# Optimization experiments

Hardware: AMD Instinct MI355X
Metric: run time of the kernel (lower is better)

The kernel has to match this reference:

```python
import jax, jax.numpy as jnp
import numpy as np

B, S, E, H = 2, 2048, 1024, 16
D = E // H  # head_dim = 64

def setup_inputs() -> dict:
    key = jax.random.key(0)
    ks = jax.random.split(key, 11)
    s = 1.0 / np.sqrt(E)
    inp = {
        'query': jax.random.normal(ks[0], (B, S, E), jnp.float32),
        'key':   jax.random.normal(ks[1], (B, S, E), jnp.float32),
        'value': jax.random.normal(ks[2], (B, S, E), jnp.float32),
        'Wq': jax.random.uniform(ks[3], (E, E), jnp.float32, -s, s),
        'bq': jax.random.uniform(ks[4], (E,), jnp.float32, -s, s),
        'Wk': jax.random.uniform(ks[5], (E, E), jnp.float32, -s, s),
        'bk': jax.random.uniform(ks[6], (E,), jnp.float32, -s, s),
        'Wv': jax.random.uniform(ks[7], (E, E), jnp.float32, -s, s),
        'bv': jax.random.uniform(ks[8], (E,), jnp.float32, -s, s),
        'Wo': jax.random.uniform(ks[9], (E, E), jnp.float32, -s, s),
        'bo': jax.random.uniform(ks[10], (E,), jnp.float32, -s, s),
    }
    return inp

def reference(query, key, value, Wq, bq, Wk, bk, Wv, bv, Wo, bo):
    # project and split heads: [B,S,E] -> [B,H,S,D]
    def proj(x, W, b):
        y = jnp.einsum('bse,fe->bsf', x, W) + b  # torch Linear: x @ W.T + b
        return y.reshape(B, S, H, D).transpose(0, 2, 1, 3)
    q = proj(query, Wq, bq)
    k = proj(key, Wk, bk)
    v = proj(value, Wv, bv)
    scores = jnp.einsum('bhqd,bhkd->bhqk', q, k) / jnp.sqrt(jnp.float32(D))
    attn = jax.nn.softmax(scores, axis=-1)
    out = jnp.einsum('bhqk,bhkd->bhqd', attn, v)  # [B,H,S,D]
    out = out.transpose(0, 2, 1, 3).reshape(B, S, E)
    return jnp.einsum('bse,fe->bsf', out, Wo) + bo
```

## Files before the change

kernel.cpp:

```cpp
#include <hip/hip_runtime.h>

#define B_ 2
#define S_ 2048
#define E_ 1024
#define H_ 16
#define D_ 64
#define M_ (B_*S_)
#define K_ E_

typedef __attribute__((ext_vector_type(8))) short  short8;
typedef __attribute__((ext_vector_type(4))) float  f32x4;
typedef __attribute__((ext_vector_type(8))) unsigned short u16x8;
typedef __attribute__((ext_vector_type(4))) unsigned short u16x4;
typedef __attribute__((ext_vector_type(4))) unsigned int   u32x4;

#define QSCALE 0.18033688011112042f

#if __has_builtin(__builtin_amdgcn_exp2f)
#define EXP2F(x) __builtin_amdgcn_exp2f(x)
#else
#define EXP2F(x) exp2f(x)
#endif

__device__ __forceinline__ unsigned short f2bf(float f) {
    unsigned u = __float_as_uint(f);
    u += 0x7fffu + ((u >> 16) & 1u);
    return (unsigned short)(u >> 16);
}

__device__ __forceinline__ void gl_lds16(const ushort* g, ushort* l) {
    __builtin_amdgcn_global_load_lds((const __attribute__((address_space(1))) void*)g,
                                     (__attribute__((address_space(3))) void*)l,
                                     16, 0, 0);
}

__global__ __launch_bounds__(256)
void cvt_all(const float* __restrict__ q, const float* __restrict__ k,
             const float* __restrict__ v, const float* __restrict__ wq,
             const float* __restrict__ wk, const float* __restrict__ wv,
             const float* __restrict__ wo, ushort* __restrict__ dst)
{
    const int bid = blockIdx.x;
    const float* src;
    size_t dof;
    int local;
    if (bid < 6144) {
        const int t = bid >> 11;
        src = (t == 0) ? q : (t == 1) ? k : v;
        dof = (size_t)t * 4194304u;
        local = bid & 2047;
    } else {
        const int r = bid - 6144;
        const int t = r >> 9;
        src = (t == 0) ? wq : (t == 1) ? wk : (t == 2) ? wv : wo;
        dof = 12582912u + (size_t)t * 1048576u;
        local = r & 511;
    }
    const size_t idx = (size_t)local * 2048 + threadIdx.x * 8;
    const float4 a = *(const float4*)(src + idx);
    const float4 b = *(const float4*)(src + idx + 4);
    u16x8 o;
    o[0] = f2bf(a.x); o[1] = f2bf(a.y); o[2] = f2bf(a.z); o[3] = f2bf(a.w);
    o[4] = f2bf(b.x); o[5] = f2bf(b.y); o[6] = f2bf(b.z); o[7] = f2bf(b.w);
    *(u16x8*)(dst + dof + idx) = o;
}

template<int SWAP>
__device__ __forceinline__ void gemm_core(const ushort* __restrict__ X,
                                          const ushort* __restrict__ W,
                                          int m0, int n0,
                                          f32x4 acc[4][4],
                                          ushort* Ast, ushort* Bst)
{
    const int tid  = threadIdx.x;
    const int lane = tid & 63;
    const int w    = tid >> 6;
    const int wm   = w & 1, wn = w >> 1;
    const int r0   = tid >> 2;
    const int c8   = (tid & 3) * 8;

    const f32x4 zero = {0.f, 0.f, 0.f, 0.f};
    #pragma unroll
    for (int mt = 0; mt < 4; ++mt)
        #pragma unroll
        for (int nt = 0; nt < 4; ++nt) acc[mt][nt] = zero;

    const int kb = (lane >> 4) * 8;

    for (int k0 = 0; k0 < K_; k0 += 32) {
        __syncthreads();
        const ushort* ga = X + (size_t)(m0 + r0) * K_ + k0 + c8;
        gl_lds16(ga, Ast + tid * 8);
        gl_lds16(ga + (size_t)64 * K_, Ast + 2048 + tid * 8);
        const ushort* gb = W + (size_t)(n0 + r0) * K_ + k0 + c8;
        gl_lds16(gb, Bst + tid * 8);
        gl_lds16(gb + (size_t)64 * K_, Bst + 2048 + tid * 8);
        __syncthreads();

        short8 af[4], bf[4];
        #pragma unroll
        for (int mt = 0; mt < 4; ++mt)
            af[mt] = *(const short8*)(Ast + (wm * 64 + mt * 16 + (lane & 15)) * 32 + kb);
        #pragma unroll
        for (int nt = 0; nt < 4; ++nt)
            bf[nt] = *(const short8*)(Bst + (wn * 64 + nt * 16 + (lane & 15)) * 32 + kb);
        #pragma unroll
        for (int mt = 0; mt < 4; ++mt)
            #pragma unroll
            for (int nt = 0; nt < 4; ++nt) {
                if (SWAP)
                    acc[mt][nt] = __builtin_amdgcn_mfma_f32_16x16x32_bf16(bf[nt], af[mt], acc[mt][nt], 0, 0, 0);
                else
                    acc[mt][nt] = __builtin_amdgcn_mfma_f32_16x16x32_bf16(af[mt], bf[nt], acc[mt][nt], 0, 0, 0);
            }
    }
}

__global__ __launch_bounds__(256)
void gemm_qkv(const ushort* __restrict__ Xq, const ushort* __restrict__ Xk,
              const ushort* __restrict__ Xv, const ushort* __restrict__ Wq,
              const ushort* __restrict__ Wk, const ushort* __restrict__ Wv,
              const float* __restrict__ bq, const float* __restrict__ bk,
              const float* __restrict__ bv, ushort* __restrict__ Qh,
              ushort* __restrict__ Kh, ushort* __restrict__ Vt)
{
    __shared__ ushort Ast[128 * 32];
    __shared__ ushort Bst[128 * 32];
    const int z = blockIdx.z;
    const ushort* X = (z == 0) ? Xq : (z == 1) ? Xk : Xv;
    const ushort* W = (z == 0) ? Wq : (z == 1) ? Wk : Wv;
    const float* bias = (z == 0) ? bq : (z == 1) ? bk : bv;
    ushort* dst = (z == 0) ? Qh : (z == 1) ? Kh : Vt;

    const int m0 = blockIdx.y * 128, n0 = blockIdx.x * 128;
    f32x4 acc[4][4];
    const int lane = threadIdx.x & 63, w = threadIdx.x >> 6;
    const int wm = w & 1, wn = w >> 1;
    const int l15 = lane & 15, quad = lane >> 4;

    if (z < 2) {
        gemm_core<1>(X, W, m0, n0, acc, Ast, Bst);
        const float qsc = (z == 0) ? QSCALE : 1.0f;
        #pragma unroll
        for (int nt = 0; nt < 4; ++nt) {
            const int nb = n0 + wn * 64 + nt * 16 + quad * 4;
            const int h = nb >> 6, d0 = nb & 63;
            const float4 b4 = *(const float4*)(bias + nb);
            const float bb4[4] = {b4.x, b4.y, b4.z, b4.w};
            #pragma unroll
            for (int mt = 0; mt < 4; ++mt) {
                const int tok = m0 + wm * 64 + mt * 16 + l15;
                const int b = tok >> 11, s = tok & (S_ - 1);
                u16x4 pk;
                #pragma unroll
                for (int r = 0; r < 4; ++r)
                    pk[r] = f2bf((acc[mt][nt][r] + bb4[r]) * qsc);
                *(u16x4*)&dst[(((size_t)(b * H_ + h) * S_) + s) * D_ + d0] = pk;
            }
        }
    } else {
        gemm_core<0>(X, W, m0, n0, acc, Ast, Bst);
        float bias4[4];
        #pragma unroll
        for (int nt = 0; nt < 4; ++nt)
            bias4[nt] = bias[n0 + wn * 64 + nt * 16 + l15];
        #pragma unroll
        for (int mt = 0; mt < 4; ++mt) {
            const int mrow0 = m0 + wm * 64 + mt * 16 + (quad * 4);
            const int b = mrow0 >> 11;
            const int s0 = mrow0 & (S_ - 1);
            #pragma unroll
            for (int nt = 0; nt < 4; ++nt) {
                const int n = n0 + wn * 64 + nt * 16 + l15;
                const int h = n >> 6, d = n & 63;
                u16x4 pk;
                #pragma unroll
                for (int r = 0; r < 4; ++r) pk[r] = f2bf(acc[mt][nt][r] + bias4[nt]);
                *(u16x4*)&Vt[(((size_t)(b * H_ + h) * D_) + d) * S_ + s0] = pk;
            }
        }
    }
}

__global__ __launch_bounds__(256)
void gemm_out(const ushort* __restrict__ X, const ushort* __restrict__ W,
              const float* __restrict__ bias, float* __restrict__ out)
{
    __shared__ ushort Ast[128 * 32];
    __shared__ ushort Bst[64 * 32];
    const int m0 = blockIdx.y * 128, n0 = blockIdx.x * 64;
    const int tid = threadIdx.x, lane = tid & 63, w = tid >> 6;
    const int wm = w & 1, wn = w >> 1;
    const int l15 = lane & 15, quad = lane >> 4;
    const int r0 = tid >> 2, c8 = (tid & 3) * 8;
    const int kb = quad * 8;

    const f32x4 zero = {0.f, 0.f, 0.f, 0.f};
    f32x4 acc[4][2];
    #pragma unroll
    for (int mt = 0; mt < 4; ++mt)
        #pragma unroll
        for (int nt = 0; nt < 2; ++nt) acc[mt][nt] = zero;

    for (int k0 = 0; k0 < K_; k0 += 32) {
        __syncthreads();
        const ushort* ga = X + (size_t)(m0 + r0) * K_ + k0 + c8;
        gl_lds16(ga, Ast + tid * 8);
        gl_lds16(ga + (size_t)64 * K_, Ast + 2048 + tid * 8);
        const ushort* gb = W + (size_t)(n0 + r0) * K_ + k0 + c8;
        gl_lds16(gb, Bst + tid * 8);
        __syncthreads();

        short8 af[4], bf[2];
        #pragma unroll
        for (int mt = 0; mt < 4; ++mt)
            af[mt] = *(const short8*)(Ast + (wm * 64 + mt * 16 + l15) * 32 + kb);
        #pragma unroll
        for (int nt = 0; nt < 2; ++nt)
            bf[nt] = *(const short8*)(Bst + (wn * 32 + nt * 16 + l15) * 32 + kb);
        #pragma unroll
        for (int mt = 0; mt < 4; ++mt)
            #pragma unroll
            for (int nt = 0; nt < 2; ++nt)
                acc[mt][nt] = __builtin_amdgcn_mfma_f32_16x16x32_bf16(af[mt], bf[nt], acc[mt][nt], 0, 0, 0);
    }

    float bias2[2];
    #pragma unroll
    for (int nt = 0; nt < 2; ++nt)
        bias2[nt] = bias[n0 + wn * 32 + nt * 16 + l15];

    #pragma unroll
    for (int mt = 0; mt < 4; ++mt) {
        const int mrow0 = m0 + wm * 64 + mt * 16 + quad * 4;
        #pragma unroll
        for (int nt = 0; nt < 2; ++nt) {
            const int n = n0 + wn * 32 + nt * 16 + l15;
            #pragma unroll
            for (int r = 0; r < 4; ++r)
                out[(size_t)(mrow0 + r) * E_ + n] = acc[mt][nt][r] + bias2[nt];
        }
    }
}

#define NTILE (S_ / 64)
__global__ __launch_bounds__(256, 3)
void flash_mfma(const ushort* __restrict__ Qg, const ushort* __restrict__ Kg,
                const ushort* __restrict__ Vg, ushort* __restrict__ AO)
{
    __shared__ ushort sh[20480];
    ushort* Qs = sh;
    ushort* K0 = sh + 4096;
    ushort* V0 = sh + 8192;
    ushort* K1 = sh + 12288;
    ushort* V1 = sh + 16384;

    const int tid = threadIdx.x, lane = tid & 63, w = tid >> 6;
    const int l15 = lane & 15, quad = lane >> 4;
    const int q0 = blockIdx.x * 64, h = blockIdx.y, b = blockIdx.z;
    const size_t qk_off = (size_t)(b * H_ + h) * S_ * D_;
    const size_t vt_off = (size_t)(b * H_ + h) * D_ * S_;

    #pragma unroll
    for (int i = 0; i < 2; ++i) {
        const int chunk = w + i * 4;
        const int row = chunk * 8 + (lane >> 3);
        const int gcol = (lane & 7) ^ (row & 7);
        gl_lds16(Qg + qk_off + (size_t)(q0 + row) * D_ + gcol * 8,
                 Qs + chunk * 512 + lane * 8);
        gl_lds16(Kg + qk_off + (size_t)row * D_ + gcol * 8,
                 K0 + chunk * 512 + lane * 8);
        gl_lds16(Vg + vt_off + (size_t)row * S_ + gcol * 8,
                 V0 + chunk * 512 + lane * 8);
    }
    __syncthreads();

    const f32x4 zero = {0.f, 0.f, 0.f, 0.f};
    f32x4 o[4][4];
    #pragma unroll
    for (int g = 0; g < 4; ++g)
        #pragma unroll
        for (int nt = 0; nt < 4; ++nt) o[g][nt] = zero;
    float lsum[4] = {0.f, 0.f, 0.f, 0.f};

    const int krow = (w * 16 + l15) * 64;
    const int gidx = (2 * w + (quad >> 1)) ^ (l15 & 7);

    for (int jp = 0; jp < NTILE; jp += 2) {
        short8 ka[2];
        #pragma unroll
        for (int kt = 0; kt < 2; ++kt)
            ka[kt] = *(const short8*)&K0[krow + (((kt * 4 + quad) ^ (l15 & 7)) * 8)];
        uint2 vvA[4];
        #pragma unroll
        for (int nt = 0; nt < 4; ++nt)
            vvA[nt] = *(const uint2*)&V0[(nt * 16 + l15) * 64 + gidx * 8 + (quad & 1) * 4];

        {
            const int j0n = (jp + 1) * 64;
            #pragma unroll
            for (int i = 0; i < 2; ++i) {
                const int chunk = w + i * 4;
                const int row = chunk * 8 + (lane >> 3);
                const int gcol = (lane & 7) ^ (row & 7);
                gl_lds16(Kg + qk_off + (size_t)(j0n + row) * D_ + gcol * 8,
                         K1 + chunk * 512 + lane * 8);
                gl_lds16(Vg + vt_off + (size_t)row * S_ + j0n + gcol * 8,
                         V1 + chunk * 512 + lane * 8);
            }
        }

        uint2 paLo[4];
        #pragma unroll
        for (int g = 0; g < 4; ++g) {
            const short8 qg0 = *(const short8*)&Qs[(g * 16 + l15) * 64 +
                                                   ((quad ^ (l15 & 7)) * 8)];
            const short8 qg1 = *(const short8*)&Qs[(g * 16 + l15) * 64 +
                                                   (((4 + quad) ^ (l15 & 7)) * 8)];
            f32x4 t;
            t = __builtin_amdgcn_mfma_f32_16x16x32_bf16(ka[0], qg0, zero, 0, 0, 0);
            t = __builtin_amdgcn_mfma_f32_16x16x32_bf16(ka[1], qg1, t, 0, 0, 0);
            const float p0 = EXP2F(t[0]), p1 = EXP2F(t[1]);
            const float p2 = EXP2F(t[2]), p3 = EXP2F(t[3]);
            lsum[g] += (p0 + p1) + (p2 + p3);
            const unsigned a0 = __float_as_uint(p0) + 0x8000u;
            const unsigned a1 = __float_as_uint(p1) + 0x8000u;
            const unsigned a2 = __float_as_uint(p2) + 0x8000u;
            const unsigned a3 = __float_as_uint(p3) + 0x8000u;
            paLo[g].x = (a1 & 0xffff0000u) | (a0 >> 16);
            paLo[g].y = (a3 & 0xffff0000u) | (a2 >> 16);
        }
        __syncthreads();

        #pragma unroll
        for (int kt = 0; kt < 2; ++kt)
            ka[kt] = *(const short8*)&K1[krow + (((kt * 4 + quad) ^ (l15 & 7)) * 8)];
        uint2 vvB[4];
        #pragma unroll
        for (int nt = 0; nt < 4; ++nt)
            vvB[nt] = *(const uint2*)&V1[(nt * 16 + l15) * 64 + gidx * 8 + (quad & 1) * 4];

        if (jp + 2 < NTILE) {
            const int j0n = (jp + 2) * 64;
            #pragma unroll
            for (int i = 0; i < 2; ++i) {
                const int chunk = w + i * 4;
                const int row = chunk * 8 + (lane >> 3);
                const int gcol = (lane & 7) ^ (row & 7);
                gl_lds16(Kg + qk_off + (size_t)(j0n + row) * D_ + gcol * 8,
                         K0 + chunk * 512 + lane * 8);
                gl_lds16(Vg + vt_off + (size_t)row * S_ + j0n + gcol * 8,
                         V0 + chunk * 512 + lane * 8);
            }
        }

        short8 pa8[4];
        #pragma unroll
        for (int g = 0; g < 4; ++g) {
            const short8 qg0 = *(const short8*)&Qs[(g * 16 + l15) * 64 +
                                                   ((quad ^ (l15 & 7)) * 8)];
            const short8 qg1 = *(const short8*)&Qs[(g * 16 + l15) * 64 +
                                                   (((4 + quad) ^ (l15 & 7)) * 8)];
            f32x4 t;
            t = __builtin_amdgcn_mfma_f32_16x16x32_bf16(ka[0], qg0, zero, 0, 0, 0);
            t = __builtin_amdgcn_mfma_f32_16x16x32_bf16(ka[1], qg1, t, 0, 0, 0);
            const float p0 = EXP2F(t[0]), p1 = EXP2F(t[1]);
            const float p2 = EXP2F(t[2]), p3 = EXP2F(t[3]);
            lsum[g] += (p0 + p1) + (p2 + p3);
            const unsigned a0 = __float_as_uint(p0) + 0x8000u;
            const unsigned a1 = __float_as_uint(p1) + 0x8000u;
            const unsigned a2 = __float_as_uint(p2) + 0x8000u;
            const unsigned a3 = __float_as_uint(p3) + 0x8000u;
            u32x4 pk;
            pk[0] = paLo[g].x;
            pk[1] = paLo[g].y;
            pk[2] = (a1 & 0xffff0000u) | (a0 >> 16);
            pk[3] = (a3 & 0xffff0000u) | (a2 >> 16);
            pa8[g] = __builtin_bit_cast(short8, pk);
        }

        #pragma unroll
        for (int nt = 0; nt < 4; ++nt) {
            u32x4 vk;
            vk[0] = vvA[nt].x; vk[1] = vvA[nt].y;
            vk[2] = vvB[nt].x; vk[3] = vvB[nt].y;
            const short8 vb8 = __builtin_bit_cast(short8, vk);
            #pragma unroll
            for (int g = 0; g < 4; ++g)
                o[g][nt] = __builtin_amdgcn_mfma_f32_16x16x32_bf16(pa8[g], vb8, o[g][nt], 0, 0, 0);
        }

        __syncthreads();
    }

    #pragma unroll
    for (int g = 0; g < 4; ++g) {
        lsum[g] += __shfl_xor(lsum[g], 16);
        lsum[g] += __shfl_xor(lsum[g], 32);
    }
    __syncthreads();
    float* fb = (float*)sh;
    #pragma unroll
    for (int g = 0; g < 4; ++g) {
        if (w != g) {
            #pragma unroll
            for (int nt = 0; nt < 4; ++nt)
                #pragma unroll
                for (int r = 0; r < 4; ++r)
                    fb[w * 1024 + (nt * 4 + r) * 64 + lane] = o[g][nt][r];
            if (quad == 0) fb[4096 + w * 64 + l15] = lsum[g];
        }
        __syncthreads();
        if (w == g) {
            #pragma unroll
            for (int ws = 0; ws < 4; ++ws) {
                if (ws == g) continue;
                #pragma unroll
                for (int nt = 0; nt < 4; ++nt)
                    #pragma unroll
                    for (int r = 0; r < 4; ++r)
                        o[g][nt][r] += fb[ws * 1024 + (nt * 4 + r) * 64 + lane];
                lsum[g] += fb[4096 + ws * 64 + l15];
            }
        }
        __syncthreads();
    }

    #pragma unroll
    for (int g = 0; g < 4; ++g) {
        if (w == g) {
            const float inv = 1.0f / lsum[g];
            float invr[4];
            #pragma unroll
            for (int r = 0; r < 4; ++r)
                invr[r] = __shfl(inv, (lane & 0x30) | (quad * 4 + r));
            #pragma unroll
            for (int nt = 0; nt < 4; ++nt) {
                const int e = h * 64 + nt * 16 + l15;
                #pragma unroll
                for (int r = 0; r < 4; ++r) {
                    const int s = q0 + g * 16 + quad * 4 + r;
                    AO[(size_t)(b * S_ + s) * E_ + e] = f2bf(o[g][nt][r] * invr[r]);
                }
            }
        }
    }
}

extern "C" void kernel_launch(void* const* d_in, const int* in_sizes, int n_in,
                              void* d_out, int out_size, void* d_ws, size_t ws_size,
                              hipStream_t stream) {
    const float* query = (const float*)d_in[0];
    const float* key   = (const float*)d_in[1];
    const float* value = (const float*)d_in[2];
    const float* Wq = (const float*)d_in[3];
    const float* bq = (const float*)d_in[4];
    const float* Wk = (const float*)d_in[5];
    const float* bk = (const float*)d_in[6];
    const float* Wv = (const float*)d_in[7];
    const float* bv = (const float*)d_in[8];
    const float* Wo = (const float*)d_in[9];
    const float* bo = (const float*)d_in[10];
    float* out = (float*)d_out;

    ushort* ws = (ushort*)d_ws;
    ushort* Xq  = ws;
    ushort* Xk  = ws + 4194304u;
    ushort* Xv  = ws + 8388608u;
    ushort* Wqb = ws + 12582912u;
    ushort* Wkb = ws + 13631488u;
    ushort* Wvb = ws + 14680064u;
    ushort* Wob = ws + 15728640u;
    ushort* Qh  = ws + 16777216u;
    ushort* Kh  = ws + 20971520u;
    ushort* Vt  = ws + 25165824u;
    ushort* AO  = ws + 29360128u;

    cvt_all<<<8192, 256, 0, stream>>>(query, key, value, Wq, Wk, Wv, Wo, ws);
    gemm_qkv<<<dim3(8, 32, 3), 256, 0, stream>>>(Xq, Xk, Xv, Wqb, Wkb, Wvb,
                                                 bq, bk, bv, Qh, Kh, Vt);
    flash_mfma<<<dim3(32, 16, 2), 256, 0, stream>>>(Qh, Kh, Vt, AO);
    gemm_out<<<dim3(16, 32), 256, 0, stream>>>(AO, Wob, bo, out);
}
```

Baseline: 232.5 us.

## Deepen flash attention K/V pipeline to four LDS stages with vmcnt barriers

Replaces the double-buffered K/V prefetch in the flash attention kernel with a four-stage ring buffer in LDS, issuing loads three tiles ahead. __syncthreads is replaced by explicit s_waitcnt vmcnt(N) plus s_barrier, so only the oldest stage has to land before compute. Q fragments are hoisted into registers once instead of being reread from LDS every tile. LDS use grows to about 72KB and launch bounds drop to 2 blocks per CU, which trades occupancy for deeper latency hiding.

```diff
diff --git a/kernel.cpp b/kernel.cpp
--- a/kernel.cpp
+++ b/kernel.cpp
@@ -33,6 +33,12 @@
                                      (__attribute__((address_space(3))) void*)l,
                                      16, 0, 0);
 }
+
+#define FL_SYNC(N) do {                                                   \
+    asm volatile("s_waitcnt vmcnt(" #N ")" ::: "memory");                 \
+    __builtin_amdgcn_s_barrier();                                         \
+    asm volatile("" ::: "memory");                                        \
+} while (0)
 
 __global__ __launch_bounds__(256)
 void cvt_all(const float* __restrict__ q, const float* __restrict__ k,
@@ -244,16 +250,80 @@
 }
 
 #define NTILE (S_ / 64)
-__global__ __launch_bounds__(256, 3)
+
+__device__ __forceinline__ void flash_stage(const ushort* __restrict__ Kg,
+                                            const ushort* __restrict__ Vg,
+                                            size_t qk_off, size_t vt_off,
+                                            ushort* sh, int j,
+                                            int row0, int gcol0, int row1, int gcol1,
+                                            int chunk0, int chunk1, int lane)
+{
+    ushort* sb = sh + 4096 + (j & 3) * 8192;
+    const int j0n = j * 64;
+    gl_lds16(Kg + qk_off + (size_t)(j0n + row0) * D_ + gcol0 * 8, sb + chunk0 * 512 + lane * 8);
+    gl_lds16(Vg + vt_off + (size_t)row0 * S_ + j0n + gcol0 * 8, sb + 4096 + chunk0 * 512 + lane * 8);
+    gl_lds16(Kg + qk_off + (size_t)(j0n + row1) * D_ + gcol1 * 8, sb + chunk1 * 512 + lane * 8);
+    gl_lds16(Vg + vt_off + (size_t)row1 * S_ + j0n + gcol1 * 8, sb + 4096 + chunk1 * 512 + lane * 8);
+}
+
+__device__ __forceinline__ void flash_qk(const ushort* Kb, const ushort* Vb,
+                                         const short8* qr0, const short8* qr1,
+                                         int krow, int l15, int quad, int gidx,
+                                         float* lsum, uint2* pout, uint2* vv)
+{
+    const short8 ka0 = *(const short8*)&Kb[krow + ((quad ^ (l15 & 7)) * 8)];
+    const short8 ka1 = *(const short8*)&Kb[krow + (((4 + quad) ^ (l15 & 7)) * 8)];
+    #pragma unroll
+    for (int nt = 0; nt < 4; ++nt)
+        vv[nt] = *(const uint2*)&Vb[(nt * 16 + l15) * 64 + gidx * 8 + (quad & 1) * 4];
+    const f32x4 zero = {0.f, 0.f, 0.f, 0.f};
+    #pragma unroll
+    for (int g = 0; g < 4; ++g) {
+        f32x4 t;
+        t = __builtin_amdgcn_mfma_f32_16x16x32_bf16(ka0, qr0[g], zero, 0, 0, 0);
+        t = __builtin_amdgcn_mfma_f32_16x16x32_bf16(ka1, qr1[g], t, 0, 0, 0);
+        const float p0 = EXP2F(t[0]), p1 = EXP2F(t[1]);
+        const float p2 = EXP2F(t[2]), p3 = EXP2F(t[3]);
+        lsum[g] += (p0 + p1) + (p2 + p3);
+        const unsigned a0 = __float_as_uint(p0) + 0x8000u;
+        const unsigned a1 = __float_as_uint(p1) + 0x8000u;
+        const unsigned a2 = __float_as_uint(p2) + 0x8000u;
+        const unsigned a3 = __float_as_uint(p3) + 0x8000u;
+        pout[g].x = (a1 & 0xffff0000u) | (a0 >> 16);
+        pout[g].y = (a3 & 0xffff0000u) | (a2 >> 16);
+    }
+}
+
+__device__ __forceinline__ void flash_pv(const uint2* paLo, const uint2* paHi,
+                                         const uint2* vvA, const uint2* vvB,
+                                         f32x4 o[4][4])
+{
+    short8 pa8[4];
+    #pragma unroll
+    for (int g = 0; g < 4; ++g) {
+        u32x4 pk;
+        pk[0] = paLo[g].x; pk[1] = paLo[g].y;
+        pk[2] = paHi[g].x; pk[3] = paHi[g].y;
+        pa8[g] = __builtin_bit_cast(short8, pk);
+    }
+    #pragma unroll
+    for (int nt = 0; nt < 4; ++nt) {
+        u32x4 vk;
+        vk[0] = vvA[nt].x; vk[1] = vvA[nt].y;
+        vk[2] = vvB[nt].x; vk[3] = vvB[nt].y;
+        const short8 vb8 = __builtin_bit_cast(short8, vk);
+        #pragma unroll
+        for (int g = 0; g < 4; ++g)
+            o[g][nt] = __builtin_amdgcn_mfma_f32_16x16x32_bf16(pa8[g], vb8, o[g][nt], 0, 0, 0);
+    }
+}
+
+__global__ __launch_bounds__(256, 2)
 void flash_mfma(const ushort* __restrict__ Qg, const ushort* __restrict__ Kg,
                 const ushort* __restrict__ Vg, ushort* __restrict__ AO)
 {
-    __shared__ ushort sh[20480];
+    __shared__ ushort sh[36864];
     ushort* Qs = sh;
-    ushort* K0 = sh + 4096;
-    ushort* V0 = sh + 8192;
-    ushort* K1 = sh + 12288;
-    ushort* V1 = sh + 16384;
 
     const int tid = threadIdx.x, lane = tid & 63, w = tid >> 6;
     const int l15 = lane & 15, quad = lane >> 4;
@@ -261,19 +331,26 @@
     const size_t qk_off = (size_t)(b * H_ + h) * S_ * D_;
     const size_t vt_off = (size_t)(b * H_ + h) * D_ * S_;
 
-    #pragma unroll
-    for (int i = 0; i < 2; ++i) {
-        const int chunk = w + i * 4;
-        const int row = chunk * 8 + (lane >> 3);
-        const int gcol = (lane & 7) ^ (row & 7);
-        gl_lds16(Qg + qk_off + (size_t)(q0 + row) * D_ + gcol * 8,
-                 Qs + chunk * 512 + lane * 8);
-        gl_lds16(Kg + qk_off + (size_t)row * D_ + gcol * 8,
-                 K0 + chunk * 512 + lane * 8);
-        gl_lds16(Vg + vt_off + (size_t)row * S_ + gcol * 8,
-                 V0 + chunk * 512 + lane * 8);
-    }
-    __syncthreads();
+    const int chunk0 = w, chunk1 = w + 4;
+    const int row0 = chunk0 * 8 + (lane >> 3);
+    const int row1 = chunk1 * 8 + (lane >> 3);
+    const int gcol0 = (lane & 7) ^ (row0 & 7);
+    const int gcol1 = (lane & 7) ^ (row1 & 7);
+
+    gl_lds16(Qg + qk_off + (size_t)(q0 + row0) * D_ + gcol0 * 8, Qs + chunk0 * 512 + lane * 8);
+    gl_lds16(Qg + qk_off + (size_t)(q0 + row1) * D_ + gcol1 * 8, Qs + chunk1 * 512 + lane * 8);
+    flash_stage(Kg, Vg, qk_off, vt_off, sh, 0, row0, gcol0, row1, gcol1, chunk0, chunk1, lane);
+    flash_stage(Kg, Vg, qk_off, vt_off, sh, 1, row0, gcol0, row1, gcol1, chunk0, chunk1, lane);
+    flash_stage(Kg, Vg, qk_off, vt_off, sh, 2, row0, gcol0, row1, gcol1, chunk0, chunk1, lane);
+
+    FL_SYNC(12);
+
+    short8 qr0[4], qr1[4];
+    #pragma unroll
+    for (int g = 0; g < 4; ++g) {
+        qr0[g] = *(const short8*)&Qs[(g * 16 + l15) * 64 + ((quad ^ (l15 & 7)) * 8)];
+        qr1[g] = *(const short8*)&Qs[(g * 16 + l15) * 64 + (((4 + quad) ^ (l15 & 7)) * 8)];
+    }
 
     const f32x4 zero = {0.f, 0.f, 0.f, 0.f};
     f32x4 o[4][4];
@@ -286,112 +363,39 @@
     const int krow = (w * 16 + l15) * 64;
     const int gidx = (2 * w + (quad >> 1)) ^ (l15 & 7);
 
-    for (int jp = 0; jp < NTILE; jp += 2) {
-        short8 ka[2];
-        #pragma unroll
-        for (int kt = 0; kt < 2; ++kt)
-            ka[kt] = *(const short8*)&K0[krow + (((kt * 4 + quad) ^ (l15 & 7)) * 8)];
-        uint2 vvA[4];
-        #pragma unroll
-        for (int nt = 0; nt < 4; ++nt)
-            vvA[nt] = *(const uint2*)&V0[(nt * 16 + l15) * 64 + gidx * 8 + (quad & 1) * 4];
-
+    uint2 vvA[4], vvB[4], paLo[4], paHi[4];
+
+    for (int p = 0; p < 15; ++p) {
+        const int jA = 2 * p;
+        FL_SYNC(8);
+        flash_stage(Kg, Vg, qk_off, vt_off, sh, jA + 3,
+                    row0, gcol0, row1, gcol1, chunk0, chunk1, lane);
         {
-            const int j0n = (jp + 1) * 64;
-            #pragma unroll
-            for (int i = 0; i < 2; ++i) {
-                const int chunk = w + i * 4;
-                const int row = chunk * 8 + (lane >> 3);
-                const int gcol = (lane & 7) ^ (row & 7);
-                gl_lds16(Kg + qk_off + (size_t)(j0n + row) * D_ + gcol * 8,
-                         K1 + chunk * 512 + lane * 8);
-                gl_lds16(Vg + vt_off + (size_t)row * S_ + j0n + gcol * 8,
-                         V1 + chunk * 512 + lane * 8);
-            }
-        }
-
-        uint2 paLo[4];
-        #pragma unroll
-        for (int g = 0; g < 4; ++g) {
-            const short8 qg0 = *(const short8*)&Qs[(g * 16 + l15) * 64 +
-                                                   ((quad ^ (l15 & 7)) * 8)];
-            const short8 qg1 = *(const short8*)&Qs[(g * 16 + l15) * 64 +
-                                                   (((4 + quad) ^ (l15 & 7)) * 8)];
-            f32x4 t;
-            t = __builtin_amdgcn_mfma_f32_16x16x32_bf16(ka[0], qg0, zero, 0, 0, 0);
-            t = __builtin_amdgcn_mfma_f32_16x16x32_bf16(ka[1], qg1, t, 0, 0, 0);
-            const float p0 = EXP2F(t[0]), p1 = EXP2F(t[1]);
-            const float p2 = EXP2F(t[2]), p3 = EXP2F(t[3]);
-            lsum[g] += (p0 + p1) + (p2 + p3);
-            const unsigned a0 = __float_as_uint(p0) + 0x8000u;
-            const unsigned a1 = __float_as_uint(p1) + 0x8000u;
-            const unsigned a2 = __float_as_uint(p2) + 0x8000u;
-            const unsigned a3 = __float_as_uint(p3) + 0x8000u;
-            paLo[g].x = (a1 & 0xffff0000u) | (a0 >> 16);
-            paLo[g].y = (a3 & 0xffff0000u) | (a2 >> 16);
-        }
-        __syncthreads();
-
-        #pragma unroll
-        for (int kt = 0; kt < 2; ++kt)
-            ka[kt] = *(const short8*)&K1[krow + (((kt * 4 + quad) ^ (l15 & 7)) * 8)];
-        uint2 vvB[4];
-        #pragma unroll
-        for (int nt = 0; nt < 4; ++nt)
-            vvB[nt] = *(const uint2*)&V1[(nt * 16 + l15) * 64 + gidx * 8 + (quad & 1) * 4];
-
-        if (jp + 2 < NTILE) {
-            const int j0n = (jp + 2) * 64;
-            #pragma unroll
-            for (int i = 0; i < 2; ++i) {
-                const int chunk = w + i * 4;
-                const int row = chunk * 8 + (lane >> 3);
-                const int gcol = (lane & 7) ^ (row & 7);
-                gl_lds16(Kg + qk_off + (size_t)(j0n + row) * D_ + gcol * 8,
-                         K0 + chunk * 512 + lane * 8);
-                gl_lds16(Vg + vt_off + (size_t)row * S_ + j0n + gcol * 8,
-                         V0 + chunk * 512 + lane * 8);
-            }
-        }
-
-        short8 pa8[4];
-        #pragma unroll
-        for (int g = 0; g < 4; ++g) {
-            const short8 qg0 = *(const short8*)&Qs[(g * 16 + l15) * 64 +
-                                                   ((quad ^ (l15 & 7)) * 8)];
-            const short8 qg1 = *(const short8*)&Qs[(g * 16 + l15) * 64 +
-                                                   (((4 + quad) ^ (l15 & 7)) * 8)];
-            f32x4 t;
-            t = __builtin_amdgcn_mfma_f32_16x16x32_bf16(ka[0], qg0, zero, 0, 0, 0);
-            t = __builtin_amdgcn_mfma_f32_16x16x32_bf16(ka[1], qg1, t, 0, 0, 0);
-            const float p0 = EXP2F(t[0]), p1 = EXP2F(t[1]);
-            const float p2 = EXP2F(t[2]), p3 = EXP2F(t[3]);
-            lsum[g] += (p0 + p1) + (p2 + p3);
-            const unsigned a0 = __float_as_uint(p0) + 0x8000u;
-            const unsigned a1 = __float_as_uint(p1) + 0x8000u;
-            const unsigned a2 = __float_as_uint(p2) + 0x8000u;
-            const unsigned a3 = __float_as_uint(p3) + 0x8000u;
-            u32x4 pk;
-            pk[0] = paLo[g].x;
-            pk[1] = paLo[g].y;
-            pk[2] = (a1 & 0xffff0000u) | (a0 >> 16);
-            pk[3] = (a3 & 0xffff0000u) | (a2 >> 16);
-            pa8[g] = __builtin_bit_cast(short8, pk);
-        }
-
-        #pragma unroll
-        for (int nt = 0; nt < 4; ++nt) {
-            u32x4 vk;
-            vk[0] = vvA[nt].x; vk[1] = vvA[nt].y;
-            vk[2] = vvB[nt].x; vk[3] = vvB[nt].y;
-            const short8 vb8 = __builtin_bit_cast(short8, vk);
-            #pragma unroll
-            for (int g = 0; g < 4; ++g)
-                o[g][nt] = __builtin_amdgcn_mfma_f32_16x16x32_bf16(pa8[g], vb8, o[g][nt], 0, 0, 0);
-        }
-
-        __syncthreads();
-    }
+            const ushort* KbA = sh + 4096 + (jA & 3) * 8192;
+            flash_qk(KbA, KbA + 4096, qr0, qr1, krow, l15, quad, gidx, lsum, paLo, vvA);
+        }
+        FL_SYNC(8);
+        if (jA + 4 < NTILE)
+            flash_stage(Kg, Vg, qk_off, vt_off, sh, jA + 4,
+                        row0, gcol0, row1, gcol1, chunk0, chunk1, lane);
+        {
+            const ushort* KbB = sh + 4096 + ((jA + 1) & 3) * 8192;
+            flash_qk(KbB, KbB + 4096, qr0, qr1, krow, l15, quad, gidx, lsum, paHi, vvB);
+        }
+        flash_pv(paLo, paHi, vvA, vvB, o);
+    }
+
+    FL_SYNC(4);
+    {
+        const ushort* KbA = sh + 4096 + (30 & 3) * 8192;
+        flash_qk(KbA, KbA + 4096, qr0, qr1, krow, l15, quad, gidx, lsum, paLo, vvA);
+    }
+    FL_SYNC(0);
+    {
+        const ushort* KbB = sh + 4096 + (31 & 3) * 8192;
+        flash_qk(KbB, KbB + 4096, qr0, qr1, krow, l15, quad, gidx, lsum, paHi, vvB);
+    }
+    flash_pv(paLo, paHi, vvA, vvB, o);
 
     #pragma unroll
     for (int g = 0; g < 4; ++g) {
```

Measured after the change: 231.7 us. Within noise of the previous version (-0.3%).
